# Kernel tuning notes

Measured on AMD Instinct MI355X. Metric: run time of the kernel, lower is better.

Reference implementation:

```python
import jax, jax.numpy as jnp
import numpy as np

N_CONFIGS = 8
N_NODES = 100000
N_EDGES = 400000
N_GRAPHS = 10
FEAT_DIM = 97          # 1 op-code column + 96 float features
OP_EMB = 32
MAX_OP_CODE = 128
D_IN = OP_EMB + FEAT_DIM - 1   # 128
HIDDEN = 64


def setup_inputs() -> dict:
    key = jax.random.key(0)
    ks = jax.random.split(key, 10)
    features = jax.random.normal(ks[0], (N_CONFIGS, N_NODES, FEAT_DIM), dtype=jnp.float32)
    op_codes = jax.random.randint(ks[1], (N_CONFIGS, N_NODES), 0, MAX_OP_CODE)
    features = features.at[..., 0].set(op_codes.astype(jnp.float32))
    edge_index = jax.random.randint(ks[2], (2, N_EDGES), 0, N_NODES, dtype=jnp.int32)
    lengths = jnp.full((N_GRAPHS,), N_NODES // N_GRAPHS, dtype=jnp.int32)
    s = 1.0 / np.sqrt(D_IN)
    emb_table = jax.random.normal(ks[3], (MAX_OP_CODE, OP_EMB), dtype=jnp.float32)
    W1 = jax.random.normal(ks[4], (D_IN, HIDDEN), dtype=jnp.float32) * s
    b1 = jnp.zeros((HIDDEN,), dtype=jnp.float32)
    W2 = jax.random.normal(ks[5], (HIDDEN, HIDDEN), dtype=jnp.float32) / np.sqrt(HIDDEN)
    b2 = jnp.zeros((HIDDEN,), dtype=jnp.float32)
    Wp = jax.random.normal(ks[6], (HIDDEN, 1), dtype=jnp.float32) / np.sqrt(HIDDEN)
    bp = jnp.zeros((1,), dtype=jnp.float32)
    return {"features": features, "edge_index": edge_index, "lengths": lengths,
            "emb_table": emb_table, "W1": W1, "b1": b1, "W2": W2, "b2": b2,
            "Wp": Wp, "bp": bp}


def reference(features, edge_index, lengths, emb_table, W1, b1, W2, b2, Wp, bp):
    C, N, _ = features.shape
    src, dst = edge_index[0], edge_index[1]
    # row-normalized sparse adjacency values (mean aggregation), no grad needed
    deg = jax.ops.segment_sum(jnp.ones_like(src, dtype=jnp.float32), src, num_segments=N)
    vals = 1.0 / jnp.clip(deg, 1.0)[src]              # [E]

    # embedding input layer: embed op code (col 0), concat remaining features
    op = features[..., 0].astype(jnp.int32)           # [C, N]
    x = jnp.concatenate([emb_table[op], features[..., 1:]], axis=-1)  # [C, N, D_IN]

    def spmm(h):  # (A_norm @ h) per config: out[src] += vals * h[dst]
        msg = h[:, dst, :] * vals[None, :, None]      # [C, E, D]
        return jnp.zeros((C, N, h.shape[-1]), h.dtype).at[:, src, :].add(msg)

    # message passing layers
    x = jax.nn.relu(spmm(x) @ W1 + b1)                # [C, N, HIDDEN]
    x = jax.nn.relu(spmm(x) @ W2 + b2)                # [C, N, HIDDEN]

    # projection -> per-node runtime, abs (exp=False)
    r = jnp.abs(x @ Wp + bp)                          # [C, N, 1]

    # per-graph scatter-sum pooling over nodes
    G = lengths.shape[0]
    index = jnp.repeat(jnp.arange(G), lengths, total_repeat_length=N)  # [N]
    pooled = jnp.zeros((C, G, 1), r.dtype).at[:, index, :].add(r)      # [C, G, 1]
    return jnp.squeeze(jnp.transpose(pooled, (1, 0, 2)))               # [G, C]
```

## Files before the change

### kernel.cpp

```cpp
#include <hip/hip_runtime.h>

#define NCFG 8
#define NN 100000
#define NE 400000
#define NG 10
#define FEAT 97
#define SCAN_BLOCKS 25

typedef __attribute__((ext_vector_type(8))) short bf16x8;
typedef __attribute__((ext_vector_type(4))) float f32x4;

__device__ inline short f2bf(float x){
  unsigned u = __float_as_uint(x);
  unsigned r = u + 0x7FFFu + ((u >> 16) & 1u);
  return (short)(r >> 16);
}
__device__ inline float bf2f(short h){
  return __uint_as_float(((unsigned)(unsigned short)h) << 16);
}

__global__ void k_hist(const int* __restrict__ src, int* __restrict__ deg, int e_count){
  int e = blockIdx.x*blockDim.x + threadIdx.x;
  if(e < e_count) atomicAdd(&deg[src[e]], 1);
}

__global__ __launch_bounds__(1024) void k_scanA(const int* __restrict__ deg,
    int* __restrict__ partial, int n){
  __shared__ int ws[16];
  int tid = threadIdx.x;
  int i0 = blockIdx.x*4096 + tid*4;
  int s = 0;
  #pragma unroll
  for(int i=0;i<4;i++) if(i0+i < n) s += deg[i0+i];
  #pragma unroll
  for(int off=1; off<64; off<<=1) s += __shfl_xor(s, off, 64);
  if((tid & 63) == 0) ws[tid >> 6] = s;
  __syncthreads();
  if(tid < 16){
    int v = ws[tid];
    #pragma unroll
    for(int off=1; off<16; off<<=1) v += __shfl_xor(v, off, 16);
    if(tid == 0) partial[blockIdx.x] = v;
  }
}

__global__ void k_scanB(int* __restrict__ partial, int* __restrict__ rowptr, int nb, int n){
  int tid = threadIdx.x;
  int v = (tid < nb) ? partial[tid] : 0;
  int x = v;
  #pragma unroll
  for(int off=1; off<64; off<<=1){
    int t = __shfl_up(x, off, 64);
    if(tid >= off) x += t;
  }
  if(tid < nb) partial[tid] = x - v;
  if(tid == nb-1) rowptr[n] = x;
}

__global__ __launch_bounds__(1024) void k_scanC(int* __restrict__ deg_cur,
    const int* __restrict__ partial, int* __restrict__ rowptr,
    float* __restrict__ inv_deg, int n){
  __shared__ int wsum[16];
  int tid = threadIdx.x, lane = tid & 63, w = tid >> 6;
  int i0 = blockIdx.x*4096 + tid*4;
  int v0 = (i0+0 < n) ? deg_cur[i0+0] : 0;
  int v1 = (i0+1 < n) ? deg_cur[i0+1] : 0;
  int v2 = (i0+2 < n) ? deg_cur[i0+2] : 0;
  int v3 = (i0+3 < n) ? deg_cur[i0+3] : 0;
  int s = v0+v1+v2+v3;
  int x = s;
  #pragma unroll
  for(int off=1; off<64; off<<=1){
    int t = __shfl_up(x, off, 64);
    if(lane >= off) x += t;
  }
  if(lane == 63) wsum[w] = x;
  __syncthreads();
  if(w == 0){
    int y = (lane < 16) ? wsum[lane] : 0;
    #pragma unroll
    for(int off=1; off<16; off<<=1){
      int t = __shfl_up(y, off, 64);
      if(lane >= off) y += t;
    }
    if(lane < 16) wsum[lane] = y;
  }
  __syncthreads();
  int waveoff = (w > 0) ? wsum[w-1] : 0;
  int run = partial[blockIdx.x] + waveoff + (x - s);
  if(i0+0 < n){ rowptr[i0+0]=run; deg_cur[i0+0]=run; inv_deg[i0+0]=1.0f/(float)max(v0,1); run+=v0; }
  if(i0+1 < n){ rowptr[i0+1]=run; deg_cur[i0+1]=run; inv_deg[i0+1]=1.0f/(float)max(v1,1); run+=v1; }
  if(i0+2 < n){ rowptr[i0+2]=run; deg_cur[i0+2]=run; inv_deg[i0+2]=1.0f/(float)max(v2,1); run+=v2; }
  if(i0+3 < n){ rowptr[i0+3]=run; deg_cur[i0+3]=run; inv_deg[i0+3]=1.0f/(float)max(v3,1); run+=v3; }
}

__global__ void k_fill(const int* __restrict__ src, const int* __restrict__ dst,
                       int* __restrict__ cursor, int* __restrict__ col, int e_count){
  int e = blockIdx.x*blockDim.x + threadIdx.x;
  if(e < e_count){
    int pos = atomicAdd(&cursor[src[e]], 1);
    col[pos] = dst[e];
  }
}

__global__ void k_embW1(const float* __restrict__ emb, const float* __restrict__ W1,
                        float* __restrict__ embW1){
  int o = blockIdx.x, j = threadIdx.x;
  float s = 0.f;
  #pragma unroll
  for(int k=0;k<32;k++) s += emb[o*32+k] * W1[k*64+j];
  embW1[o*64+j] = s;
}

__global__ void k_offsets(const int* __restrict__ lengths, int* __restrict__ off){
  if(threadIdx.x == 0){
    int s = 0;
    for(int g=0; g<NG; g++){ off[g] = s; s += lengths[g]; }
    off[NG] = s;
  }
}

__global__ __launch_bounds__(256) void k_prepB(const float* __restrict__ W1, const float* __restrict__ W2,
    short* __restrict__ bW1hi, short* __restrict__ bW1lo,
    short* __restrict__ bW2hi, short* __restrict__ bW2lo){
  int e = blockIdx.x*256 + threadIdx.x;
  if(e < 3*4*64*8){
    int i=e&7, l=(e>>3)&63, t=(e>>9)&3, kc=e>>11;
    int k=kc*32+((l>>4)<<3)+i, c=t*16+(l&15);
    float wv = W1[(32+k)*64+c];
    short h=f2bf(wv); bW1hi[e]=h; bW1lo[e]=f2bf(wv-bf2f(h));
  }
  if(e < 2*4*64*8){
    int i=e&7, l=(e>>3)&63, t=(e>>9)&3, kc=e>>11;
    int k=kc*32+((l>>4)<<3)+i, c=t*16+(l&15);
    float wv = W2[k*64+c];
    short h=f2bf(wv); bW2hi[e]=h; bW2lo[e]=f2bf(wv-bf2f(h));
  }
}

__global__ __launch_bounds__(256) void k_gemm1(const float* __restrict__ feat,
    const float* __restrict__ embW1,
    const short* __restrict__ bW1hi, const short* __restrict__ bW1lo,
    unsigned short* __restrict__ z_all){
  __shared__ float lds_f[64*FEAT];
  int tid = threadIdx.x;
  int nb = blockIdx.x * 64;
  int cfg = blockIdx.y;
  const float* gsrc = feat + ((size_t)cfg*NN + nb)*FEAT;

  if(nb + 64 <= NN){
    for(int idx = tid; idx < 1552; idx += 256)
      *(float4*)&lds_f[idx*4] = *(const float4*)(gsrc + idx*4);
  } else {
    int nvalid = (NN - nb)*FEAT;
    for(int idx = tid; idx < 1552; idx += 256){
      int base = idx*4;
      float4 v;
      v.x = (base+0 < nvalid) ? gsrc[base+0] : 0.f;
      v.y = (base+1 < nvalid) ? gsrc[base+1] : 0.f;
      v.z = (base+2 < nvalid) ? gsrc[base+2] : 0.f;
      v.w = (base+3 < nvalid) ? gsrc[base+3] : 0.f;
      *(float4*)&lds_f[base] = v;
    }
  }
  __syncthreads();

  int w = tid >> 6, l = tid & 63;
  int node_loc = w*16 + (l & 15);
  int g8 = (l >> 4) << 3;

  f32x4 acc[4] = {{0,0,0,0},{0,0,0,0},{0,0,0,0},{0,0,0,0}};
  #pragma unroll
  for(int kc = 0; kc < 3; kc++){
    const float* ap = &lds_f[node_loc*FEAT + 1 + g8 + kc*32];
    bf16x8 bfeat;
    #pragma unroll
    for(int i=0;i<8;i++) bfeat[i] = f2bf(ap[i]);
    #pragma unroll
    for(int t=0;t<4;t++){
      const bf16x8 ah = *(const bf16x8*)&bW1hi[((kc*4 + t)*64 + l)*8];
      const bf16x8 al = *(const bf16x8*)&bW1lo[((kc*4 + t)*64 + l)*8];
      acc[t] = __builtin_amdgcn_mfma_f32_16x16x32_bf16(ah, bfeat, acc[t], 0,0,0);
      acc[t] = __builtin_amdgcn_mfma_f32_16x16x32_bf16(al, bfeat, acc[t], 0,0,0);
    }
  }
  int node = nb + node_loc;
  int g = l >> 4;
  if(node < NN){
    int op = (int)lds_f[node_loc*FEAT];
    unsigned short* zrow = z_all + ((size_t)node*NCFG + cfg)*64;
    #pragma unroll
    for(int t=0;t<4;t++){
      int f0 = t*16 + g*4;
      const float4 e = *(const float4*)&embW1[op*64 + f0];
      ushort4 pk;
      pk.x = (unsigned short)f2bf(acc[t][0] + e.x);
      pk.y = (unsigned short)f2bf(acc[t][1] + e.y);
      pk.z = (unsigned short)f2bf(acc[t][2] + e.z);
      pk.w = (unsigned short)f2bf(acc[t][3] + e.w);
      *(ushort4*)(zrow + f0) = pk;
    }
  }
}

__global__ __launch_bounds__(256) void k_gather1(const int* __restrict__ rowptr,
    const int* __restrict__ col, const float* __restrict__ inv_deg,
    const unsigned short* __restrict__ z_all, const float* __restrict__ b1,
    unsigned short* __restrict__ h_all){
  int tid = threadIdx.x, lane = tid & 63;
  int n = (blockIdx.x << 2) + (tid >> 6);
  if(n >= NN) return;
  int sub = lane & 7;
  const unsigned short* zl = z_all + lane*8;
  int kb = rowptr[n], ke = rowptr[n+1];
  float a0[8]={0,0,0,0,0,0,0,0}, a1[8]={0,0,0,0,0,0,0,0};
  float a2[8]={0,0,0,0,0,0,0,0}, a3[8]={0,0,0,0,0,0,0,0};
  int k = kb;
  for(; k+4 <= ke; k += 4){
    int d0=col[k], d1=col[k+1], d2=col[k+2], d3=col[k+3];
    const bf16x8 v0 = *(const bf16x8*)(zl + (size_t)d0*512);
    const bf16x8 v1 = *(const bf16x8*)(zl + (size_t)d1*512);
    const bf16x8 v2 = *(const bf16x8*)(zl + (size_t)d2*512);
    const bf16x8 v3 = *(const bf16x8*)(zl + (size_t)d3*512);
    #pragma unroll
    for(int i=0;i<8;i++){
      a0[i] += bf2f(v0[i]); a1[i] += bf2f(v1[i]);
      a2[i] += bf2f(v2[i]); a3[i] += bf2f(v3[i]);
    }
  }
  for(; k < ke; k++){
    int d = col[k];
    const bf16x8 v = *(const bf16x8*)(zl + (size_t)d*512);
    #pragma unroll
    for(int i=0;i<8;i++) a0[i] += bf2f(v[i]);
  }
  float inv = inv_deg[n];
  const float4 bA = *(const float4*)(b1 + sub*8);
  const float4 bB = *(const float4*)(b1 + sub*8 + 4);
  float bv[8] = {bA.x,bA.y,bA.z,bA.w,bB.x,bB.y,bB.z,bB.w};
  bf16x8 o;
  #pragma unroll
  for(int i=0;i<8;i++){
    float acc = (a0[i]+a1[i]) + (a2[i]+a3[i]);
    o[i] = f2bf(fmaxf(fmaf(acc, inv, bv[i]), 0.f));
  }
  *(bf16x8*)(h_all + (size_t)n*512 + lane*8) = o;
}

__global__ __launch_bounds__(256) void k_gather2W(const int* __restrict__ rowptr,
    const int* __restrict__ col, const float* __restrict__ inv_deg,
    const unsigned short* __restrict__ h_all,
    const short* __restrict__ bW2hi, const short* __restrict__ bW2lo,
    const float* __restrict__ b2, const float* __restrict__ Wp,
    const float* __restrict__ bp, float* __restrict__ r_all){
  __shared__ unsigned short V[128][68];
  int tid = threadIdx.x, lane = tid & 63, w = tid >> 6;
  int nb = blockIdx.x * 16;
  int cfg = lane >> 3, sub = lane & 7;
  const unsigned short* hl = h_all + lane*8;

  for(int i = 0; i < 4; i++){
    int nl = w*4 + i;
    int n = nb + nl;
    int kb = rowptr[n], ke = rowptr[n+1];
    float a0[8]={0,0,0,0,0,0,0,0}, a1[8]={0,0,0,0,0,0,0,0};
    float a2[8]={0,0,0,0,0,0,0,0}, a3[8]={0,0,0,0,0,0,0,0};
    int k = kb;
    for(; k+4 <= ke; k += 4){
      int d0=col[k], d1=col[k+1], d2=col[k+2], d3=col[k+3];
      const bf16x8 v0 = *(const bf16x8*)(hl + (size_t)d0*512);
      const bf16x8 v1 = *(const bf16x8*)(hl + (size_t)d1*512);
      const bf16x8 v2 = *(const bf16x8*)(hl + (size_t)d2*512);
      const bf16x8 v3 = *(const bf16x8*)(hl + (size_t)d3*512);
      #pragma unroll
      for(int j=0;j<8;j++){
        a0[j] += bf2f(v0[j]); a1[j] += bf2f(v1[j]);
        a2[j] += bf2f(v2[j]); a3[j] += bf2f(v3[j]);
      }
    }
    for(; k < ke; k++){
      int d = col[k];
      const bf16x8 v = *(const bf16x8*)(hl + (size_t)d*512);
      #pragma unroll
      for(int j=0;j<8;j++) a0[j] += bf2f(v[j]);
    }
    float inv = inv_deg[n];
    bf16x8 o;
    #pragma unroll
    for(int j=0;j<8;j++){
      float acc = (a0[j]+a1[j]) + (a2[j]+a3[j]);
      o[j] = f2bf(acc * inv);
    }
    *(bf16x8*)&V[nl*8 + cfg][sub*8] = o;
  }
  __syncthreads();

  float bp0 = bp[0];
  int cb = lane & 15;
  int koff = (lane >> 4) << 3;
  #pragma unroll
  for(int at = 0; at < 2; at++){
    int tile = w*2 + at;
    int trow = tile*16 + cb;
    f32x4 acc[4] = {{0,0,0,0},{0,0,0,0},{0,0,0,0},{0,0,0,0}};
    #pragma unroll
    for(int kc = 0; kc < 2; kc++){
      const bf16x8 a = *(const bf16x8*)&V[trow][kc*32 + koff];
      #pragma unroll
      for(int t=0;t<4;t++){
        const bf16x8 bh = *(const bf16x8*)&bW2hi[((kc*4+t)*64 + lane)*8];
        const bf16x8 bl = *(const bf16x8*)&bW2lo[((kc*4+t)*64 + lane)*8];
        acc[t] = __builtin_amdgcn_mfma_f32_16x16x32_bf16(a, bh, acc[t], 0,0,0);
        acc[t] = __builtin_amdgcn_mfma_f32_16x16x32_bf16(a, bl, acc[t], 0,0,0);
      }
    }
    float part[4];
    #pragma unroll
    for(int j=0;j<4;j++){
      float p = 0.f;
      #pragma unroll
      for(int t=0;t<4;t++){
        int c = t*16 + cb;
        p += fmaxf(acc[t][j] + b2[c], 0.f) * Wp[c];
      }
      part[j] = p;
    }
    #pragma unroll
    for(int off=1; off<16; off<<=1){
      #pragma unroll
      for(int j=0;j<4;j++) part[j] += __shfl_xor(part[j], off, 64);
    }
    if(cb == 0){
      #pragma unroll
      for(int j=0;j<4;j++){
        int row = tile*16 + ((lane>>4)<<2) + j;
        int node = nb + (row >> 3);
        int cfgo = row & 7;
        r_all[(size_t)cfgo*NN + node] = fabsf(part[j] + bp0);
      }
    }
  }
}

__global__ __launch_bounds__(256) void k_pool(const float* __restrict__ r_all,
    const int* __restrict__ off, float* __restrict__ out){
  __shared__ float red[256];
  int b = blockIdx.x;
  int g = b >> 3, c = b & 7;
  int lo = off[g], hi = off[g+1];
  float s = 0.f;
  for(int i = lo + (int)threadIdx.x; i < hi; i += 256) s += r_all[(size_t)c*NN + i];
  red[threadIdx.x] = s;
  __syncthreads();
  for(int w=128; w>0; w>>=1){
    if((int)threadIdx.x < w) red[threadIdx.x] += red[threadIdx.x + w];
    __syncthreads();
  }
  if(threadIdx.x == 0) out[b] = red[0];
}

extern "C" void kernel_launch(void* const* d_in, const int* in_sizes, int n_in,
                              void* d_out, int out_size, void* d_ws, size_t ws_size,
                              hipStream_t stream){
  (void)in_sizes; (void)n_in; (void)out_size; (void)ws_size;
  const float* feat = (const float*)d_in[0];
  const int*   eidx = (const int*)d_in[1];
  const int*   lens = (const int*)d_in[2];
  const float* emb  = (const float*)d_in[3];
  const float* W1   = (const float*)d_in[4];
  const float* b1   = (const float*)d_in[5];
  const float* W2   = (const float*)d_in[6];
  const float* b2   = (const float*)d_in[7];
  const float* Wp   = (const float*)d_in[8];
  const float* bp   = (const float*)d_in[9];
  float* out = (float*)d_out;
  const int* src = eidx;
  const int* dst = eidx + NE;

  char* ws = (char*)d_ws;
  size_t o = 0;
  auto alloc = [&](size_t bytes)->char*{ char* p = ws + o; o = (o + bytes + 255) & ~(size_t)255; return p; };
  int*   rowptr  = (int*)  alloc((NN+1)*4);
  int*   cursor  = (int*)  alloc((size_t)NN*4);
  int*   colx    = (int*)  alloc((size_t)NE*4);
  float* invd    = (float*)alloc((size_t)NN*4);
  int*   goff    = (int*)  alloc((NG+1)*4);
  int*   spart   = (int*)  alloc(SCAN_BLOCKS*4);
  float* eW1     = (float*)alloc(128*64*4);
  short* bW1hi   = (short*)alloc(3*4*64*8*2);
  short* bW1lo   = (short*)alloc(3*4*64*8*2);
  short* bW2hi   = (short*)alloc(2*4*64*8*2);
  short* bW2lo   = (short*)alloc(2*4*64*8*2);
  float* r_all   = (float*)alloc((size_t)NCFG*NN*4);
  unsigned short* z_all = (unsigned short*)alloc((size_t)NN*NCFG*64*2);
  unsigned short* h_all = (unsigned short*)alloc((size_t)NN*NCFG*64*2);

  hipMemsetAsync(cursor, 0, (size_t)NN*4, stream);
  k_hist   <<<(NE+255)/256, 256, 0, stream>>>(src, cursor, NE);
  k_scanA  <<<SCAN_BLOCKS, 1024, 0, stream>>>(cursor, spart, NN);
  k_scanB  <<<1, 64, 0, stream>>>(spart, rowptr, SCAN_BLOCKS, NN);
  k_scanC  <<<SCAN_BLOCKS, 1024, 0, stream>>>(cursor, spart, rowptr, invd, NN);
  k_fill   <<<(NE+255)/256, 256, 0, stream>>>(src, dst, cursor, colx, NE);
  k_embW1  <<<128, 64, 0, stream>>>(emb, W1, eW1);
  k_prepB  <<<24, 256, 0, stream>>>(W1, W2, bW1hi, bW1lo, bW2hi, bW2lo);
  k_offsets<<<1, 64, 0, stream>>>(lens, goff);

  dim3 ggemm((NN+63)/64, NCFG);
  k_gemm1  <<<ggemm, 256, 0, stream>>>(feat, eW1, bW1hi, bW1lo, z_all);
  k_gather1<<<(NN+3)/4, 256, 0, stream>>>(rowptr, colx, invd, z_all, b1, h_all);
  k_gather2W<<<NN/16, 256, 0, stream>>>(rowptr, colx, invd, h_all, bW2hi, bW2lo, b2, Wp, bp, r_all);
  k_pool   <<<NCFG*NG, 256, 0, stream>>>(r_all, goff, out);
}
```

Baseline: 367.0 us.

## Process configs in two halves to shrink gather working set and prefetch features

```diff
diff --git a/kernel.cpp b/kernel.cpp
--- a/kernel.cpp
+++ b/kernel.cpp
@@ -8,6 +8,7 @@
 #define SCAN_BLOCKS 25
 
 typedef __attribute__((ext_vector_type(8))) short bf16x8;
+typedef __attribute__((ext_vector_type(4))) short bf16x4;
 typedef __attribute__((ext_vector_type(4))) float f32x4;
 
 __device__ inline short f2bf(float x){
@@ -103,104 +104,124 @@
   }
 }
 
-__global__ void k_embW1(const float* __restrict__ emb, const float* __restrict__ W1,
-                        float* __restrict__ embW1){
-  int o = blockIdx.x, j = threadIdx.x;
-  float s = 0.f;
-  #pragma unroll
-  for(int k=0;k<32;k++) s += emb[o*32+k] * W1[k*64+j];
-  embW1[o*64+j] = s;
-}
-
-__global__ void k_offsets(const int* __restrict__ lengths, int* __restrict__ off){
-  if(threadIdx.x == 0){
-    int s = 0;
-    for(int g=0; g<NG; g++){ off[g] = s; s += lengths[g]; }
-    off[NG] = s;
-  }
-}
-
-__global__ __launch_bounds__(256) void k_prepB(const float* __restrict__ W1, const float* __restrict__ W2,
+__global__ __launch_bounds__(256) void k_prep(const float* __restrict__ emb,
+    const float* __restrict__ W1, const float* __restrict__ W2,
+    const int* __restrict__ lengths, float* __restrict__ embW1,
     short* __restrict__ bW1hi, short* __restrict__ bW1lo,
-    short* __restrict__ bW2hi, short* __restrict__ bW2lo){
-  int e = blockIdx.x*256 + threadIdx.x;
-  if(e < 3*4*64*8){
-    int i=e&7, l=(e>>3)&63, t=(e>>9)&3, kc=e>>11;
-    int k=kc*32+((l>>4)<<3)+i, c=t*16+(l&15);
-    float wv = W1[(32+k)*64+c];
-    short h=f2bf(wv); bW1hi[e]=h; bW1lo[e]=f2bf(wv-bf2f(h));
-  }
-  if(e < 2*4*64*8){
-    int i=e&7, l=(e>>3)&63, t=(e>>9)&3, kc=e>>11;
-    int k=kc*32+((l>>4)<<3)+i, c=t*16+(l&15);
-    float wv = W2[k*64+c];
-    short h=f2bf(wv); bW2hi[e]=h; bW2lo[e]=f2bf(wv-bf2f(h));
+    short* __restrict__ bW2hi, short* __restrict__ bW2lo, int* __restrict__ goff){
+  int b = blockIdx.x, tid = threadIdx.x;
+  if(b < 128){
+    if(tid < 64){
+      float s = 0.f;
+      #pragma unroll
+      for(int k=0;k<32;k++) s += emb[b*32+k] * W1[k*64+tid];
+      embW1[b*64+tid] = s;
+    }
+  } else if(b < 152){
+    int e = (b-128)*256 + tid;
+    {
+      int i=e&7, l=(e>>3)&63, t=(e>>9)&3, kc=e>>11;
+      int k=kc*32+((l>>4)<<3)+i, c=t*16+(l&15);
+      float wv = W1[(32+k)*64+c];
+      short h=f2bf(wv); bW1hi[e]=h; bW1lo[e]=f2bf(wv-bf2f(h));
+    }
+    if(e < 4096){
+      int i=e&7, l=(e>>3)&63, t=(e>>9)&3, kc=e>>11;
+      int k=kc*32+((l>>4)<<3)+i, c=t*16+(l&15);
+      float wv = W2[k*64+c];
+      short h=f2bf(wv); bW2hi[e]=h; bW2lo[e]=f2bf(wv-bf2f(h));
+    }
+  } else {
+    if(tid == 0){
+      int s = 0;
+      for(int g=0; g<NG; g++){ goff[g] = s; s += lengths[g]; }
+      goff[NG] = s;
+    }
   }
 }
 
 __global__ __launch_bounds__(256) void k_gemm1(const float* __restrict__ feat,
     const float* __restrict__ embW1,
     const short* __restrict__ bW1hi, const short* __restrict__ bW1lo,
-    unsigned short* __restrict__ z_all){
+    unsigned short* __restrict__ z_all, int c0){
   __shared__ float lds_f[64*FEAT];
   int tid = threadIdx.x;
   int nb = blockIdx.x * 64;
-  int cfg = blockIdx.y;
-  const float* gsrc = feat + ((size_t)cfg*NN + nb)*FEAT;
-
-  if(nb + 64 <= NN){
-    for(int idx = tid; idx < 1552; idx += 256)
-      *(float4*)&lds_f[idx*4] = *(const float4*)(gsrc + idx*4);
-  } else {
-    int nvalid = (NN - nb)*FEAT;
-    for(int idx = tid; idx < 1552; idx += 256){
-      int base = idx*4;
-      float4 v;
-      v.x = (base+0 < nvalid) ? gsrc[base+0] : 0.f;
-      v.y = (base+1 < nvalid) ? gsrc[base+1] : 0.f;
-      v.z = (base+2 < nvalid) ? gsrc[base+2] : 0.f;
-      v.w = (base+3 < nvalid) ? gsrc[base+3] : 0.f;
-      *(float4*)&lds_f[base] = v;
-    }
-  }
-  __syncthreads();
-
   int w = tid >> 6, l = tid & 63;
   int node_loc = w*16 + (l & 15);
-  int g8 = (l >> 4) << 3;
-
-  f32x4 acc[4] = {{0,0,0,0},{0,0,0,0},{0,0,0,0},{0,0,0,0}};
-  #pragma unroll
-  for(int kc = 0; kc < 3; kc++){
-    const float* ap = &lds_f[node_loc*FEAT + 1 + g8 + kc*32];
-    bf16x8 bfeat;
-    #pragma unroll
-    for(int i=0;i<8;i++) bfeat[i] = f2bf(ap[i]);
-    #pragma unroll
-    for(int t=0;t<4;t++){
-      const bf16x8 ah = *(const bf16x8*)&bW1hi[((kc*4 + t)*64 + l)*8];
-      const bf16x8 al = *(const bf16x8*)&bW1lo[((kc*4 + t)*64 + l)*8];
-      acc[t] = __builtin_amdgcn_mfma_f32_16x16x32_bf16(ah, bfeat, acc[t], 0,0,0);
-      acc[t] = __builtin_amdgcn_mfma_f32_16x16x32_bf16(al, bfeat, acc[t], 0,0,0);
-    }
-  }
-  int node = nb + node_loc;
   int g = l >> 4;
-  if(node < NN){
-    int op = (int)lds_f[node_loc*FEAT];
-    unsigned short* zrow = z_all + ((size_t)node*NCFG + cfg)*64;
-    #pragma unroll
-    for(int t=0;t<4;t++){
-      int f0 = t*16 + g*4;
-      const float4 e = *(const float4*)&embW1[op*64 + f0];
-      ushort4 pk;
-      pk.x = (unsigned short)f2bf(acc[t][0] + e.x);
-      pk.y = (unsigned short)f2bf(acc[t][1] + e.y);
-      pk.z = (unsigned short)f2bf(acc[t][2] + e.z);
-      pk.w = (unsigned short)f2bf(acc[t][3] + e.w);
-      *(ushort4*)(zrow + f0) = pk;
-    }
-  }
+  int g8 = g << 3;
+  bool full = (nb + 64 <= NN);
+
+  float4 st[7];
+  #define LOADREGS(c) { \
+    const float* gp = feat + ((size_t)(c)*NN + nb)*FEAT; \
+    _Pragma("unroll") \
+    for(int i=0;i<6;i++) st[i] = *(const float4*)(gp + (tid + i*256)*4); \
+    if(tid < 16) st[6] = *(const float4*)(gp + (tid + 1536)*4); \
+  }
+  #define WRITELDS() { \
+    _Pragma("unroll") \
+    for(int i=0;i<6;i++) *(float4*)&lds_f[(tid + i*256)*4] = st[i]; \
+    if(tid < 16) *(float4*)&lds_f[(tid + 1536)*4] = st[6]; \
+  }
+
+  if(full) LOADREGS(c0);
+
+  for(int cc = 0; cc < 4; cc++){
+    __syncthreads();
+    if(full){
+      WRITELDS();
+      if(cc < 3) LOADREGS(c0+cc+1);
+    } else {
+      const float* gp = feat + ((size_t)(c0+cc)*NN + nb)*FEAT;
+      int nvalid = (NN - nb)*FEAT;
+      for(int idx = tid; idx < 1552; idx += 256){
+        int base = idx*4;
+        float4 v;
+        v.x = (base+0 < nvalid) ? gp[base+0] : 0.f;
+        v.y = (base+1 < nvalid) ? gp[base+1] : 0.f;
+        v.z = (base+2 < nvalid) ? gp[base+2] : 0.f;
+        v.w = (base+3 < nvalid) ? gp[base+3] : 0.f;
+        *(float4*)&lds_f[base] = v;
+      }
+    }
+    __syncthreads();
+
+    f32x4 acc[4] = {{0,0,0,0},{0,0,0,0},{0,0,0,0},{0,0,0,0}};
+    #pragma unroll
+    for(int kc = 0; kc < 3; kc++){
+      const float* ap = &lds_f[node_loc*FEAT + 1 + g8 + kc*32];
+      bf16x8 bfeat;
+      #pragma unroll
+      for(int i=0;i<8;i++) bfeat[i] = f2bf(ap[i]);
+      #pragma unroll
+      for(int t=0;t<4;t++){
+        const bf16x8 ah = *(const bf16x8*)&bW1hi[((kc*4 + t)*64 + l)*8];
+        const bf16x8 al = *(const bf16x8*)&bW1lo[((kc*4 + t)*64 + l)*8];
+        acc[t] = __builtin_amdgcn_mfma_f32_16x16x32_bf16(ah, bfeat, acc[t], 0,0,0);
+        acc[t] = __builtin_amdgcn_mfma_f32_16x16x32_bf16(al, bfeat, acc[t], 0,0,0);
+      }
+    }
+    int node = nb + node_loc;
+    if(node < NN){
+      int op = (int)lds_f[node_loc*FEAT];
+      unsigned short* zrow = z_all + ((size_t)node*4 + cc)*64;
+      #pragma unroll
+      for(int t=0;t<4;t++){
+        int f0 = t*16 + g*4;
+        const float4 e = *(const float4*)&embW1[op*64 + f0];
+        ushort4 pk;
+        pk.x = (unsigned short)f2bf(acc[t][0] + e.x);
+        pk.y = (unsigned short)f2bf(acc[t][1] + e.y);
+        pk.z = (unsigned short)f2bf(acc[t][2] + e.z);
+        pk.w = (unsigned short)f2bf(acc[t][3] + e.w);
+        *(ushort4*)(zrow + f0) = pk;
+      }
+    }
+  }
+  #undef LOADREGS
+  #undef WRITELDS
 }
 
 __global__ __launch_bounds__(256) void k_gather1(const int* __restrict__ rowptr,
@@ -210,41 +231,39 @@
   int tid = threadIdx.x, lane = tid & 63;
   int n = (blockIdx.x << 2) + (tid >> 6);
   if(n >= NN) return;
-  int sub = lane & 7;
-  const unsigned short* zl = z_all + lane*8;
+  int sub = lane & 15;
+  const unsigned short* zl = z_all + lane*4;
   int kb = rowptr[n], ke = rowptr[n+1];
-  float a0[8]={0,0,0,0,0,0,0,0}, a1[8]={0,0,0,0,0,0,0,0};
-  float a2[8]={0,0,0,0,0,0,0,0}, a3[8]={0,0,0,0,0,0,0,0};
+  float a0[4]={0,0,0,0}, a1[4]={0,0,0,0}, a2[4]={0,0,0,0}, a3[4]={0,0,0,0};
   int k = kb;
   for(; k+4 <= ke; k += 4){
     int d0=col[k], d1=col[k+1], d2=col[k+2], d3=col[k+3];
-    const bf16x8 v0 = *(const bf16x8*)(zl + (size_t)d0*512);
-    const bf16x8 v1 = *(const bf16x8*)(zl + (size_t)d1*512);
-    const bf16x8 v2 = *(const bf16x8*)(zl + (size_t)d2*512);
-    const bf16x8 v3 = *(const bf16x8*)(zl + (size_t)d3*512);
-    #pragma unroll
-    for(int i=0;i<8;i++){
+    const bf16x4 v0 = *(const bf16x4*)(zl + (size_t)d0*256);
+    const bf16x4 v1 = *(const bf16x4*)(zl + (size_t)d1*256);
+    const bf16x4 v2 = *(const bf16x4*)(zl + (size_t)d2*256);
+    const bf16x4 v3 = *(const bf16x4*)(zl + (size_t)d3*256);
+    #pragma unroll
+    for(int i=0;i<4;i++){
       a0[i] += bf2f(v0[i]); a1[i] += bf2f(v1[i]);
       a2[i] += bf2f(v2[i]); a3[i] += bf2f(v3[i]);
     }
   }
   for(; k < ke; k++){
     int d = col[k];
-    const bf16x8 v = *(const bf16x8*)(zl + (size_t)d*512);
-    #pragma unroll
-    for(int i=0;i<8;i++) a0[i] += bf2f(v[i]);
+    const bf16x4 v = *(const bf16x4*)(zl + (size_t)d*256);
+    #pragma unroll
+    for(int i=0;i<4;i++) a0[i] += bf2f(v[i]);
   }
   float inv = inv_deg[n];
-  const float4 bA = *(const float4*)(b1 + sub*8);
-  const float4 bB = *(const float4*)(b1 + sub*8 + 4);
-  float bv[8] = {bA.x,bA.y,bA.z,bA.w,bB.x,bB.y,bB.z,bB.w};
-  bf16x8 o;
-  #pragma unroll
-  for(int i=0;i<8;i++){
+  const float4 b = *(const float4*)(b1 + sub*4);
+  float bv[4] = {b.x,b.y,b.z,b.w};
+  bf16x4 o;
+  #pragma unroll
+  for(int i=0;i<4;i++){
     float acc = (a0[i]+a1[i]) + (a2[i]+a3[i]);
     o[i] = f2bf(fmaxf(fmaf(acc, inv, bv[i]), 0.f));
   }
-  *(bf16x8*)(h_all + (size_t)n*512 + lane*8) = o;
+  *(bf16x4*)(h_all + (size_t)n*256 + lane*4) = o;
 }
 
 __global__ __launch_bounds__(256) void k_gather2W(const int* __restrict__ rowptr,
@@ -252,92 +271,87 @@
     const unsigned short* __restrict__ h_all,
     const short* __restrict__ bW2hi, const short* __restrict__ bW2lo,
     const float* __restrict__ b2, const float* __restrict__ Wp,
-    const float* __restrict__ bp, float* __restrict__ r_all){
-  __shared__ unsigned short V[128][68];
+    const float* __restrict__ bp, float* __restrict__ r_all, int c0){
+  __shared__ unsigned short V[64][68];
   int tid = threadIdx.x, lane = tid & 63, w = tid >> 6;
   int nb = blockIdx.x * 16;
-  int cfg = lane >> 3, sub = lane & 7;
-  const unsigned short* hl = h_all + lane*8;
+  int cc = lane >> 4, sub = lane & 15;
+  const unsigned short* hl = h_all + lane*4;
 
   for(int i = 0; i < 4; i++){
     int nl = w*4 + i;
     int n = nb + nl;
     int kb = rowptr[n], ke = rowptr[n+1];
-    float a0[8]={0,0,0,0,0,0,0,0}, a1[8]={0,0,0,0,0,0,0,0};
-    float a2[8]={0,0,0,0,0,0,0,0}, a3[8]={0,0,0,0,0,0,0,0};
+    float a0[4]={0,0,0,0}, a1[4]={0,0,0,0}, a2[4]={0,0,0,0}, a3[4]={0,0,0,0};
     int k = kb;
     for(; k+4 <= ke; k += 4){
       int d0=col[k], d1=col[k+1], d2=col[k+2], d3=col[k+3];
-      const bf16x8 v0 = *(const bf16x8*)(hl + (size_t)d0*512);
-      const bf16x8 v1 = *(const bf16x8*)(hl + (size_t)d1*512);
-      const bf16x8 v2 = *(const bf16x8*)(hl + (size_t)d2*512);
-      const bf16x8 v3 = *(const bf16x8*)(hl + (size_t)d3*512);
-      #pragma unroll
-      for(int j=0;j<8;j++){
+      const bf16x4 v0 = *(const bf16x4*)(hl + (size_t)d0*256);
+      const bf16x4 v1 = *(const bf16x4*)(hl + (size_t)d1*256);
+      const bf16x4 v2 = *(const bf16x4*)(hl + (size_t)d2*256);
+      const bf16x4 v3 = *(const bf16x4*)(hl + (size_t)d3*256);
+      #pragma unroll
+      for(int j=0;j<4;j++){
         a0[j] += bf2f(v0[j]); a1[j] += bf2f(v1[j]);
         a2[j] += bf2f(v2[j]); a3[j] += bf2f(v3[j]);
       }
     }
     for(; k < ke; k++){
       int d = col[k];
-      const bf16x8 v = *(const bf16x8*)(hl + (size_t)d*512);
-      #pragma unroll
-      for(int j=0;j<8;j++) a0[j] += bf2f(v[j]);
+      const bf16x4 v = *(const bf16x4*)(hl + (size_t)d*256);
+      #pragma unroll
+      for(int j=0;j<4;j++) a0[j] += bf2f(v[j]);
     }
     float inv = inv_deg[n];
-    bf16x8 o;
-    #pragma unroll
-    for(int j=0;j<8;j++){
+    bf16x4 o;
+    #pragma unroll
+    for(int j=0;j<4;j++){
       float acc = (a0[j]+a1[j]) + (a2[j]+a3[j]);
       o[j] = f2bf(acc * inv);
     }
-    *(bf16x8*)&V[nl*8 + cfg][sub*8] = o;
+    *(bf16x4*)&V[nl*4 + cc][sub*4] = o;
   }
   __syncthreads();
 
   float bp0 = bp[0];
   int cb = lane & 15;
   int koff = (lane >> 4) << 3;
-  #pragma unroll
-  for(int at = 0; at < 2; at++){
-    int tile = w*2 + at;
-    int trow = tile*16 + cb;
-    f32x4 acc[4] = {{0,0,0,0},{0,0,0,0},{0,0,0,0},{0,0,0,0}};
-    #pragma unroll
-    for(int kc = 0; kc < 2; kc++){
-      const bf16x8 a = *(const bf16x8*)&V[trow][kc*32 + koff];
-      #pragma unroll
-      for(int t=0;t<4;t++){
-        const bf16x8 bh = *(const bf16x8*)&bW2hi[((kc*4+t)*64 + lane)*8];
-        const bf16x8 bl = *(const bf16x8*)&bW2lo[((kc*4+t)*64 + lane)*8];
-        acc[t] = __builtin_amdgcn_mfma_f32_16x16x32_bf16(a, bh, acc[t], 0,0,0);
-        acc[t] = __builtin_amdgcn_mfma_f32_16x16x32_bf16(a, bl, acc[t], 0,0,0);
-      }
-    }
-    float part[4];
+  int trow = w*16 + cb;
+  f32x4 acc[4] = {{0,0,0,0},{0,0,0,0},{0,0,0,0},{0,0,0,0}};
+  #pragma unroll
+  for(int kc = 0; kc < 2; kc++){
+    const bf16x8 a = *(const bf16x8*)&V[trow][kc*32 + koff];
+    #pragma unroll
+    for(int t=0;t<4;t++){
+      const bf16x8 bh = *(const bf16x8*)&bW2hi[((kc*4+t)*64 + lane)*8];
+      const bf16x8 bl = *(const bf16x8*)&bW2lo[((kc*4+t)*64 + lane)*8];
+      acc[t] = __builtin_amdgcn_mfma_f32_16x16x32_bf16(a, bh, acc[t], 0,0,0);
+      acc[t] = __builtin_amdgcn_mfma_f32_16x16x32_bf16(a, bl, acc[t], 0,0,0);
+    }
+  }
+  float part[4];
+  #pragma unroll
+  for(int j=0;j<4;j++){
+    float p = 0.f;
+    #pragma unroll
+    for(int t=0;t<4;t++){
+      int c = t*16 + cb;
+      p += fmaxf(acc[t][j] + b2[c], 0.f) * Wp[c];
+    }
+    part[j] = p;
+  }
+  #pragma unroll
+  for(int off=1; off<16; off<<=1){
+    #pragma unroll
+    for(int j=0;j<4;j++) part[j] += __shfl_xor(part[j], off, 64);
+  }
+  if(cb == 0){
     #pragma unroll
     for(int j=0;j<4;j++){
-      float p = 0.f;
-      #pragma unroll
-      for(int t=0;t<4;t++){
-        int c = t*16 + cb;
-        p += fmaxf(acc[t][j] + b2[c], 0.f) * Wp[c];
-      }
-      part[j] = p;
-    }
-    #pragma unroll
-    for(int off=1; off<16; off<<=1){
-      #pragma unroll
-      for(int j=0;j<4;j++) part[j] += __shfl_xor(part[j], off, 64);
-    }
-    if(cb == 0){
-      #pragma unroll
-      for(int j=0;j<4;j++){
-        int row = tile*16 + ((lane>>4)<<2) + j;
-        int node = nb + (row >> 3);
-        int cfgo = row & 7;
-        r_all[(size_t)cfgo*NN + node] = fabsf(part[j] + bp0);
-      }
+      int row = w*16 + ((lane>>4)<<2) + j;
+      int node = nb + (row >> 2);
+      int cfgo = c0 + (row & 3);
+      r_all[(size_t)cfgo*NN + node] = fabsf(part[j] + bp0);
     }
   }
 }
@@ -392,22 +406,21 @@
   short* bW2hi   = (short*)alloc(2*4*64*8*2);
   short* bW2lo   = (short*)alloc(2*4*64*8*2);
   float* r_all   = (float*)alloc((size_t)NCFG*NN*4);
-  unsigned short* z_all = (unsigned short*)alloc((size_t)NN*NCFG*64*2);
-  unsigned short* h_all = (unsigned short*)alloc((size_t)NN*NCFG*64*2);
+  unsigned short* z_all = (unsigned short*)alloc((size_t)NN*4*64*2);
+  unsigned short* h_all = (unsigned short*)alloc((size_t)NN*4*64*2);
 
   hipMemsetAsync(cursor, 0, (size_t)NN*4, stream);
-  k_hist   <<<(NE+255)/256, 256, 0, stream>>>(src, cursor, NE);
-  k_scanA  <<<SCAN_BLOCKS, 1024, 0, stream>>>(cursor, spart, NN);
-  k_scanB  <<<1, 64, 0, stream>>>(spart, rowptr, SCAN_BLOCKS, NN);
-  k_scanC  <<<SCAN_BLOCKS, 1024, 0, stream>>>(cursor, spart, rowptr, invd, NN);
-  k_fill   <<<(NE+255)/256, 256, 0, stream>>>(src, dst, cursor, colx, NE);
-  k_embW1  <<<128, 64, 0, stream>>>(emb, W1, eW1);
-  k_prepB  <<<24, 256, 0, stream>>>(W1, W2, bW1hi, bW1lo, bW2hi, bW2lo);
-  k_offsets<<<1, 64, 0, stream>>>(lens, goff);
-
-  dim3 ggemm((NN+63)/64, NCFG);
-  k_gemm1  <<<ggemm, 256, 0, stream>>>(feat, eW1, bW1hi, bW1lo, z_all);
-  k_gather1<<<(NN+3)/4, 256, 0, stream>>>(rowptr, colx, invd, z_all, b1, h_all);
-  k_gather2W<<<NN/16, 256, 0, stream>>>(rowptr, colx, invd, h_all, bW2hi, bW2lo, b2, Wp, bp, r_all);
-  k_pool   <<<NCFG*NG, 256, 0, stream>>>(r_all, goff, out);
-}
+  k_hist  <<<(NE+255)/256, 256, 0, stream>>>(src, cursor, NE);
+  k_scanA <<<SCAN_BLOCKS, 1024, 0, stream>>>(cursor, spart, NN);
+  k_scanB <<<1, 64, 0, stream>>>(spart, rowptr, SCAN_BLOCKS, NN);
+  k_scanC <<<SCAN_BLOCKS, 1024, 0, stream>>>(cursor, spart, rowptr, invd, NN);
+  k_fill  <<<(NE+255)/256, 256, 0, stream>>>(src, dst, cursor, colx, NE);
+  k_prep  <<<153, 256, 0, stream>>>(emb, W1, W2, lens, eW1, bW1hi, bW1lo, bW2hi, bW2lo, goff);
+
+  for(int c0 = 0; c0 < NCFG; c0 += 4){
+    k_gemm1   <<<(NN+63)/64, 256, 0, stream>>>(feat, eW1, bW1hi, bW1lo, z_all, c0);
+    k_gather1 <<<(NN+3)/4, 256, 0, stream>>>(rowptr, colx, invd, z_all, b1, h_all);
+    k_gather2W<<<NN/16, 256, 0, stream>>>(rowptr, colx, invd, h_all, bW2hi, bW2lo, b2, Wp, bp, r_all, c0);
+  }
+  k_pool<<<NCFG*NG, 256, 0, stream>>>(r_all, goff, out);
+}
```

Measured after the change: 525.9 us. 43.3% more time.
